# Kernel optimization log

Hardware: AMD Instinct MI355X
Metric: run time of the kernel (lower is better)

The kernel has to match this reference:

```python
import jax, jax.numpy as jnp
import numpy as np

B, NL, NP, E = 64, 128, 128, 4096


def setup_inputs() -> dict:
    key = jax.random.key(0)
    k1, k2, k3, k4, k5 = jax.random.split(key, 5)
    P = jax.random.uniform(k1, (B, NL, NP), dtype=jnp.float32)
    # normalize rows so P looks like soft assignment probabilities
    P = P / P.sum(-1, keepdims=True)
    d_error = jax.random.uniform(k2, (NP, NP), dtype=jnp.float32)
    edge_weights = jax.random.uniform(k3, (B, E), dtype=jnp.float32)
    d_hw = jax.random.randint(k4, (NP, NP), 0, 6, dtype=jnp.int32)
    edge_pairs = jax.random.randint(k5, (B, E, 2), 0, NL, dtype=jnp.int64)
    return {"P": P, "d_error": d_error, "edge_weights": edge_weights,
            "d_hw": d_hw, "edge_pairs": edge_pairs}


def reference(P, d_error, edge_weights, d_hw, edge_pairs):
    # A_fidelity = adjacency (d_hw == 1) weighted by clamped fidelity
    A_fid = (d_hw == 1).astype(P.dtype) * jnp.maximum(1.0 - d_error, 0.0)  # [Np,Np]
    i = edge_pairs[..., 0]  # [B,E]
    j = edge_pairs[..., 1]  # [B,E]
    Pi = jnp.take_along_axis(P, i[..., None], axis=1)  # [B,E,Np] gather of P[b,i,:]
    Pj = jnpp = jnp.take_along_axis(P, j[..., None], axis=1)  # [B,E,Np]
    # per-edge score: P[b,i,:] @ A_fid @ P[b,j,:]
    scores = jnp.einsum('bep,pq,beq->be', Pi, A_fid, Pj)
    w_sum = jnp.maximum(edge_weights.sum(-1), 1e-8)  # [B]
    sample_adj = (edge_weights * scores).sum(-1) / w_sum  # [B]
    # all samples have edges -> valid_samples == B
    loss = -sample_adj.mean()
    return loss
```

## Files before the change

kernel.cpp:

```cpp
#include <hip/hip_runtime.h>
#include <hip/hip_bf16.h>

#define B_   64
#define NL_  128
#define NP_  128
#define E_   4096


__global__ __launch_bounds__(256) void k_prep(
    const float* __restrict__ d_error,
    const int*   __restrict__ d_hw,
    const float* __restrict__ ew,
    float* __restrict__ A,
    float* __restrict__ den)
{
    const int b = blockIdx.x;
    const int t = threadIdx.x;

    int idx = b * 256 + t;
    float a = 0.0f;
    if (d_hw[idx] == 1) a = fmaxf(1.0f - d_error[idx], 0.0f);
    A[idx] = a;

    const float4* ew4 = (const float4*)(ew + b * E_);
    float s = 0.0f;
    #pragma unroll
    for (int k = 0; k < 4; ++k) {
        float4 v = ew4[k * 256 + t];
        s += v.x + v.y + v.z + v.w;
    }
    #pragma unroll
    for (int off = 32; off >= 1; off >>= 1) s += __shfl_xor(s, off, 64);
    __shared__ float rs[4];
    if ((t & 63) == 0) rs[t >> 6] = s;
    __syncthreads();
    if (t == 0) den[b] = rs[0] + rs[1] + rs[2] + rs[3];
}

__global__ __launch_bounds__(256) void k_main(
    const float* __restrict__ P,
    const float* __restrict__ A,
    const float* __restrict__ ew,
    const int*   __restrict__ pairs_raw,
    float* __restrict__ num_part)
{
    __shared__ float Plds[NL_ * NP_];
    __shared__ float WT[NL_ * 16];
    __shared__ float red[4];

    const int b     = blockIdx.x >> 3;
    const int chunk = blockIdx.x & 7;
    const int r0    = chunk * 16;
    const int t  = threadIdx.x;
    const int tr = t >> 5;
    const int tc = t & 31;

    float4* WT4 = (float4*)WT;
    WT4[2*t]     = float4{0,0,0,0};
    WT4[2*t + 1] = float4{0,0,0,0};

    const float4* Pg4 = (const float4*)(P + (size_t)b * NL_ * NP_);
    float4* Pl4 = (float4*)Plds;
    #pragma unroll
    for (int k = 0; k < 16; ++k) {
        int f = k * 256 + t;
        Pl4[f] = Pg4[f];
    }
    __syncthreads();

    int hw = pairs_raw[2 * (t & 63) + 1];
    unsigned long long nz = __ballot(hw != 0);
    const int is64 = (nz == 0ULL);

    const float* wrow = ew + (size_t)b * E_;
    if (is64) {
        const int4* pp = (const int4*)pairs_raw + (size_t)b * E_;
        #pragma unroll 4
        for (int k = 0; k < 16; ++k) {
            int e = k * 256 + t;
            int4 pr = pp[e];
            int i = pr.x, j = pr.z;
            if (i >= r0 && i < r0 + 16)
                atomicAdd(&WT[j * 16 + (i - r0)], wrow[e]);
        }
    } else {
        const int2* pp = (const int2*)pairs_raw + (size_t)b * E_;
        #pragma unroll 4
        for (int k = 0; k < 16; ++k) {
            int e = k * 256 + t;
            int2 pr = pp[e];
            int i = pr.x, j = pr.y;
            if (i >= r0 && i < r0 + 16)
                atomicAdd(&WT[j * 16 + (i - r0)], wrow[e]);
        }
    }

    const float* Pr0 = P + ((size_t)b * NL_ + r0 + 2*tr) * NP_;
    const float* Pr1 = Pr0 + NP_;
    const float4* A4 = (const float4*)A;
    float4 q0 = {0,0,0,0}, q1 = {0,0,0,0};
    #pragma unroll 8
    for (int p = 0; p < NP_; ++p) {
        float4 av = A4[p * 32 + tc];
        float pv0 = Pr0[p];
        float pv1 = Pr1[p];
        q0.x = fmaf(pv0, av.x, q0.x); q0.y = fmaf(pv0, av.y, q0.y);
        q0.z = fmaf(pv0, av.z, q0.z); q0.w = fmaf(pv0, av.w, q0.w);
        q1.x = fmaf(pv1, av.x, q1.x); q1.y = fmaf(pv1, av.y, q1.y);
        q1.z = fmaf(pv1, av.z, q1.z); q1.w = fmaf(pv1, av.w, q1.w);
    }
    __syncthreads();

    float4 racc0 = {0,0,0,0}, racc1 = {0,0,0,0};
    const float2* WT2 = (const float2*)WT;
    const float4* Pl4r = (const float4*)Plds;
    #pragma unroll 8
    for (int lp = 0; lp < NL_; ++lp) {
        float2 w01 = WT2[lp * 8 + tr];
        float4 pv  = Pl4r[lp * 32 + tc];
        racc0.x = fmaf(w01.x, pv.x, racc0.x); racc0.y = fmaf(w01.x, pv.y, racc0.y);
        racc0.z = fmaf(w01.x, pv.z, racc0.z); racc0.w = fmaf(w01.x, pv.w, racc0.w);
        racc1.x = fmaf(w01.y, pv.x, racc1.x); racc1.y = fmaf(w01.y, pv.y, racc1.y);
        racc1.z = fmaf(w01.y, pv.z, racc1.z); racc1.w = fmaf(w01.y, pv.w, racc1.w);
    }

    float nacc = q0.x*racc0.x + q0.y*racc0.y + q0.z*racc0.z + q0.w*racc0.w
               + q1.x*racc1.x + q1.y*racc1.y + q1.z*racc1.z + q1.w*racc1.w;
    #pragma unroll
    for (int off = 32; off >= 1; off >>= 1) nacc += __shfl_xor(nacc, off, 64);
    if ((t & 63) == 0) red[t >> 6] = nacc;
    __syncthreads();
    if (t == 0) num_part[blockIdx.x] = red[0] + red[1] + red[2] + red[3];
}

__global__ __launch_bounds__(64) void k_final(
    const float* __restrict__ num_part,
    const float* __restrict__ den,
    float* __restrict__ out)
{
    int b = threadIdx.x;
    float n = 0.0f;
    #pragma unroll
    for (int c = 0; c < 8; ++c) n += num_part[b * 8 + c];
    float v = n / fmaxf(den[b], 1e-8f);
    #pragma unroll
    for (int off = 32; off >= 1; off >>= 1) v += __shfl_xor(v, off, 64);
    if (b == 0) out[0] = -v / (float)B_;
}

extern "C" void kernel_launch(void* const* d_in, const int* in_sizes, int n_in,
                              void* d_out, int out_size, void* d_ws, size_t ws_size,
                              hipStream_t stream) {
    const float* P       = (const float*)d_in[0];
    const float* d_error = (const float*)d_in[1];
    const float* ew      = (const float*)d_in[2];
    const int*   d_hw    = (const int*)d_in[3];
    const int*   pairs   = (const int*)d_in[4];
    float* out = (float*)d_out;

    char*  ws  = (char*)d_ws;
    float* A   = (float*)ws;
    float* num = (float*)(ws + 65536);
    float* den = (float*)(ws + 65536 + 2048);

    k_prep <<<64,  256, 0, stream>>>(d_error, d_hw, ew, A, den);
    k_main <<<512, 256, 0, stream>>>(P, A, ew, pairs, num);
    k_final<<<1,   64,  0, stream>>>(num, den, out);
}
```

Baseline: 96.99 us.

## Scatter edge weights into global W matrix in prep kernel, drop LDS staging

Moves the edge-weight scatter out of the main kernel into the prep kernel, which builds a full per-batch 128x128 weight matrix in global memory with global atomics. Previously every one of the 8 chunk blocks read all 4096 edges, so each edge was re-read and filtered 8 times. The main kernel now reads W and P straight from global/L2 instead of staging P in 64KB of LDS, which should raise occupancy. In exchange it adds a 4MB memset, global atomic contention, and an extra 4MB round trip through L2/HBM.

```diff
diff --git a/kernel.cpp b/kernel.cpp
--- a/kernel.cpp
+++ b/kernel.cpp
@@ -11,43 +11,66 @@
     const float* __restrict__ d_error,
     const int*   __restrict__ d_hw,
     const float* __restrict__ ew,
+    const int*   __restrict__ pairs_raw,
     float* __restrict__ A,
+    float* __restrict__ Wt,
     float* __restrict__ den)
 {
-    const int b = blockIdx.x;
-    const int t = threadIdx.x;
+    const int blk  = blockIdx.x;
+    const int b    = blk >> 1;
+    const int half = blk & 1;
+    const int t    = threadIdx.x;
 
-    int idx = b * 256 + t;
-    float a = 0.0f;
-    if (d_hw[idx] == 1) a = fmaxf(1.0f - d_error[idx], 0.0f);
-    A[idx] = a;
+    if (t < 128) {
+        int idx = blk * 128 + t;
+        A[idx] = (d_hw[idx] == 1) ? fmaxf(1.0f - d_error[idx], 0.0f) : 0.0f;
+    }
 
-    const float4* ew4 = (const float4*)(ew + b * E_);
-    float s = 0.0f;
-    #pragma unroll
-    for (int k = 0; k < 4; ++k) {
-        float4 v = ew4[k * 256 + t];
-        s += v.x + v.y + v.z + v.w;
+    int hwv = pairs_raw[2 * (t & 63) + 1];
+    unsigned long long nz = __ballot(hwv != 0);
+    const int is64 = (nz == 0ULL);
+
+    const float* wrow = ew + (size_t)b * E_ + half * 2048;
+
+    {
+        const float4* ew4 = (const float4*)wrow;
+        float4 v0 = ew4[t];
+        float4 v1 = ew4[t + 256];
+        float s = v0.x + v0.y + v0.z + v0.w + v1.x + v1.y + v1.z + v1.w;
+        #pragma unroll
+        for (int off = 32; off >= 1; off >>= 1) s += __shfl_xor(s, off, 64);
+        __shared__ float rs[4];
+        if ((t & 63) == 0) rs[t >> 6] = s;
+        __syncthreads();
+        if (t == 0) atomicAdd(&den[b], rs[0] + rs[1] + rs[2] + rs[3]);
     }
-    #pragma unroll
-    for (int off = 32; off >= 1; off >>= 1) s += __shfl_xor(s, off, 64);
-    __shared__ float rs[4];
-    if ((t & 63) == 0) rs[t >> 6] = s;
-    __syncthreads();
-    if (t == 0) den[b] = rs[0] + rs[1] + rs[2] + rs[3];
+
+    float* Wb = Wt + (size_t)b * (NL_ * NL_);
+    if (is64) {
+        const int4* pp = (const int4*)pairs_raw + (size_t)b * E_ + half * 2048;
+        #pragma unroll 4
+        for (int k = 0; k < 8; ++k) {
+            int e = k * 256 + t;
+            int4 pr = pp[e];
+            atomicAdd(&Wb[pr.z * NL_ + pr.x], wrow[e]);
+        }
+    } else {
+        const int2* pp = (const int2*)pairs_raw + (size_t)b * E_ + half * 2048;
+        #pragma unroll 4
+        for (int k = 0; k < 8; ++k) {
+            int e = k * 256 + t;
+            int2 pr = pp[e];
+            atomicAdd(&Wb[pr.y * NL_ + pr.x], wrow[e]);
+        }
+    }
 }
 
 __global__ __launch_bounds__(256) void k_main(
     const float* __restrict__ P,
     const float* __restrict__ A,
-    const float* __restrict__ ew,
-    const int*   __restrict__ pairs_raw,
+    const float* __restrict__ Wt,
     float* __restrict__ num_part)
 {
-    __shared__ float Plds[NL_ * NP_];
-    __shared__ float WT[NL_ * 16];
-    __shared__ float red[4];
-
     const int b     = blockIdx.x >> 3;
     const int chunk = blockIdx.x & 7;
     const int r0    = chunk * 16;
@@ -55,48 +78,10 @@
     const int tr = t >> 5;
     const int tc = t & 31;
 
-    float4* WT4 = (float4*)WT;
-    WT4[2*t]     = float4{0,0,0,0};
-    WT4[2*t + 1] = float4{0,0,0,0};
+    const float* Pb  = P + (size_t)b * NL_ * NP_;
+    const float* Pr0 = Pb + (size_t)(r0 + 2*tr) * NP_;
+    const float* Pr1 = Pr0 + NP_;
 
-    const float4* Pg4 = (const float4*)(P + (size_t)b * NL_ * NP_);
-    float4* Pl4 = (float4*)Plds;
-    #pragma unroll
-    for (int k = 0; k < 16; ++k) {
-        int f = k * 256 + t;
-        Pl4[f] = Pg4[f];
-    }
-    __syncthreads();
-
-    int hw = pairs_raw[2 * (t & 63) + 1];
-    unsigned long long nz = __ballot(hw != 0);
-    const int is64 = (nz == 0ULL);
-
-    const float* wrow = ew + (size_t)b * E_;
-    if (is64) {
-        const int4* pp = (const int4*)pairs_raw + (size_t)b * E_;
-        #pragma unroll 4
-        for (int k = 0; k < 16; ++k) {
-            int e = k * 256 + t;
-            int4 pr = pp[e];
-            int i = pr.x, j = pr.z;
-            if (i >= r0 && i < r0 + 16)
-                atomicAdd(&WT[j * 16 + (i - r0)], wrow[e]);
-        }
-    } else {
-        const int2* pp = (const int2*)pairs_raw + (size_t)b * E_;
-        #pragma unroll 4
-        for (int k = 0; k < 16; ++k) {
-            int e = k * 256 + t;
-            int2 pr = pp[e];
-            int i = pr.x, j = pr.y;
-            if (i >= r0 && i < r0 + 16)
-                atomicAdd(&WT[j * 16 + (i - r0)], wrow[e]);
-        }
-    }
-
-    const float* Pr0 = P + ((size_t)b * NL_ + r0 + 2*tr) * NP_;
-    const float* Pr1 = Pr0 + NP_;
     const float4* A4 = (const float4*)A;
     float4 q0 = {0,0,0,0}, q1 = {0,0,0,0};
     #pragma unroll 8
@@ -109,25 +94,26 @@
         q1.x = fmaf(pv1, av.x, q1.x); q1.y = fmaf(pv1, av.y, q1.y);
         q1.z = fmaf(pv1, av.z, q1.z); q1.w = fmaf(pv1, av.w, q1.w);
     }
-    __syncthreads();
 
-    float4 racc0 = {0,0,0,0}, racc1 = {0,0,0,0};
-    const float2* WT2 = (const float2*)WT;
-    const float4* Pl4r = (const float4*)Plds;
+    const float2* W2 = (const float2*)(Wt + (size_t)b * (NL_ * NL_));
+    const float4* P4 = (const float4*)Pb;
+    const int wof = (r0 >> 1) + tr;
+    float4 ra0 = {0,0,0,0}, ra1 = {0,0,0,0};
     #pragma unroll 8
     for (int lp = 0; lp < NL_; ++lp) {
-        float2 w01 = WT2[lp * 8 + tr];
-        float4 pv  = Pl4r[lp * 32 + tc];
-        racc0.x = fmaf(w01.x, pv.x, racc0.x); racc0.y = fmaf(w01.x, pv.y, racc0.y);
-        racc0.z = fmaf(w01.x, pv.z, racc0.z); racc0.w = fmaf(w01.x, pv.w, racc0.w);
-        racc1.x = fmaf(w01.y, pv.x, racc1.x); racc1.y = fmaf(w01.y, pv.y, racc1.y);
-        racc1.z = fmaf(w01.y, pv.z, racc1.z); racc1.w = fmaf(w01.y, pv.w, racc1.w);
+        float2 w01 = W2[lp * 64 + wof];
+        float4 pv  = P4[lp * 32 + tc];
+        ra0.x = fmaf(w01.x, pv.x, ra0.x); ra0.y = fmaf(w01.x, pv.y, ra0.y);
+        ra0.z = fmaf(w01.x, pv.z, ra0.z); ra0.w = fmaf(w01.x, pv.w, ra0.w);
+        ra1.x = fmaf(w01.y, pv.x, ra1.x); ra1.y = fmaf(w01.y, pv.y, ra1.y);
+        ra1.z = fmaf(w01.y, pv.z, ra1.z); ra1.w = fmaf(w01.y, pv.w, ra1.w);
     }
 
-    float nacc = q0.x*racc0.x + q0.y*racc0.y + q0.z*racc0.z + q0.w*racc0.w
-               + q1.x*racc1.x + q1.y*racc1.y + q1.z*racc1.z + q1.w*racc1.w;
+    float nacc = q0.x*ra0.x + q0.y*ra0.y + q0.z*ra0.z + q0.w*ra0.w
+               + q1.x*ra1.x + q1.y*ra1.y + q1.z*ra1.z + q1.w*ra1.w;
     #pragma unroll
     for (int off = 32; off >= 1; off >>= 1) nacc += __shfl_xor(nacc, off, 64);
+    __shared__ float red[4];
     if ((t & 63) == 0) red[t >> 6] = nacc;
     __syncthreads();
     if (t == 0) num_part[blockIdx.x] = red[0] + red[1] + red[2] + red[3];
@@ -159,11 +145,14 @@
     float* out = (float*)d_out;
 
     char*  ws  = (char*)d_ws;
-    float* A   = (float*)ws;
-    float* num = (float*)(ws + 65536);
-    float* den = (float*)(ws + 65536 + 2048);
+    float* Wt  = (float*)ws;
+    float* den = (float*)(ws + 4194304);
+    float* num = (float*)(ws + 4194560);
+    float* A   = (float*)(ws + 4196608);
 
-    k_prep <<<64,  256, 0, stream>>>(d_error, d_hw, ew, A, den);
-    k_main <<<512, 256, 0, stream>>>(P, A, ew, pairs, num);
+    hipMemsetAsync(ws, 0, 4194560, stream);
+
+    k_prep <<<128, 256, 0, stream>>>(d_error, d_hw, ew, pairs, A, Wt, den);
+    k_main <<<512, 256, 0, stream>>>(P, A, Wt, num);
     k_final<<<1,   64,  0, stream>>>(num, den, out);
 }
```

Measured after the change: 107.6 us. 1.11x slower.
